# Kernel optimization log

Hardware: AMD Instinct MI355X
Metric: run time of the kernel (lower is better)

## Reference

```python
import jax, jax.numpy as jnp
import numpy as np

N_NODES = 100000
N_EDGES = 1600000
D_IN = 128
D_EMB = 128


def setup_inputs() -> dict:
    key = jax.random.key(0)
    ks = jax.random.split(key, 8)
    x = jax.random.normal(ks[0], (N_NODES, D_IN), dtype=jnp.float32)
    src = jax.random.randint(ks[1], (N_EDGES,), 0, N_NODES, dtype=jnp.int32)
    dst = jax.random.randint(ks[2], (N_EDGES,), 0, N_NODES, dtype=jnp.int32)
    # Glorot-ish init for GraphConv weights
    s = 1.0 / np.sqrt(D_EMB)
    W0 = jax.random.normal(ks[3], (D_IN, D_EMB), dtype=jnp.float32) * s
    W1 = jax.random.normal(ks[4], (D_EMB, D_EMB), dtype=jnp.float32) * s
    W2 = jax.random.normal(ks[5], (D_EMB, D_EMB), dtype=jnp.float32) * s
    b0 = jnp.zeros((D_EMB,), jnp.float32)
    b1 = jnp.zeros((D_EMB,), jnp.float32)
    b2 = jnp.zeros((D_EMB,), jnp.float32)
    return {"x": x, "src": src, "dst": dst,
            "W0": W0, "b0": b0, "W1": W1, "b1": b1, "W2": W2, "b2": b2}


def _graph_conv(h, src, dst, norm_src, norm_dst, W, b):
    # DGL GraphConv, norm='both': D_out^{-1/2} A D_in^{-1/2} H W + b
    h = h * norm_src[:, None]                       # scale src features
    m = jax.ops.segment_sum(h[src], dst, num_segments=N_NODES)  # SpMM aggregate
    m = m * norm_dst[:, None]
    return m @ W + b


def reference(x, src, dst, W0, b0, W1, b1, W2, b2):
    ones = jnp.ones((N_EDGES,), jnp.float32)
    out_deg = jax.ops.segment_sum(ones, src, num_segments=N_NODES)
    in_deg = jax.ops.segment_sum(ones, dst, num_segments=N_NODES)
    norm_src = jax.lax.rsqrt(jnp.clip(out_deg, 1.0))
    norm_dst = jax.lax.rsqrt(jnp.clip(in_deg, 1.0))

    h = x
    Ws = (W0, W1, W2)
    bs = (b0, b1, b2)
    n_layers = len(Ws)
    for layer in range(n_layers):
        h = _graph_conv(h, src, dst, norm_src, norm_dst, Ws[layer], bs[layer])
        if layer != n_layers - 1:
            h = jax.nn.relu(h)  # dropout is identity in eval mode
    return h
```

## Files before the change

### kernel.cpp

```cpp
#include <hip/hip_runtime.h>
#include <hip/hip_bf16.h>

#define N_NODES 100000
#define N_EDGES 1600000
#define D 128
#define NB 1563
#define PB 512
#define CHUNK 3125
#define SCANL (NB * PB)
#define SGRID (SCANL / 512)
#define SENT N_NODES
#define ECAP_PAD (N_EDGES + 256 * NB)
#define BCAP 2816

typedef __attribute__((ext_vector_type(8))) short bf16x8;
typedef __attribute__((ext_vector_type(4))) float f32x4;

__device__ __forceinline__ float bf2f(unsigned short u) {
    unsigned int x = ((unsigned int)u) << 16;
    return __builtin_bit_cast(float, x);
}
__device__ __forceinline__ unsigned short f2bf(float f) {
    unsigned int x = __builtin_bit_cast(unsigned int, f);
    x += 0x7fffu + ((x >> 16) & 1u);
    return (unsigned short)(x >> 16);
}
__device__ __forceinline__ void accum8(float* acc, uint4 x) {
    acc[0] += bf2f((unsigned short)x.x); acc[1] += bf2f((unsigned short)(x.x >> 16));
    acc[2] += bf2f((unsigned short)x.y); acc[3] += bf2f((unsigned short)(x.y >> 16));
    acc[4] += bf2f((unsigned short)x.z); acc[5] += bf2f((unsigned short)(x.z >> 16));
    acc[6] += bf2f((unsigned short)x.w); acc[7] += bf2f((unsigned short)(x.w >> 16));
}
__device__ __forceinline__ int XP(int b) { return ((b & 7) << 6) | (b >> 3); }

__global__ __launch_bounds__(1024) void k_pcount(const int* __restrict__ src, const int* __restrict__ dst,
                                                 int* __restrict__ cntD, int* __restrict__ cntS) {
    __shared__ int hd[NB];
    __shared__ int hs[NB];
    int t = threadIdx.x, blk = blockIdx.x;
    int col = XP(blk);
    for (int i = t; i < NB; i += 1024) { hd[i] = 0; hs[i] = 0; }
    __syncthreads();
    int base = blk * CHUNK;
    for (int i = t; i < CHUNK; i += 1024) {
        int e = base + i;
        atomicAdd(&hd[dst[e] >> 6], 1);
        atomicAdd(&hs[src[e] >> 6], 1);
    }
    __syncthreads();
    for (int i = t; i < NB; i += 1024) {
        cntD[i * PB + col] = hd[i];
        cntS[i * PB + col] = hs[i];
    }
}

__global__ void k_scanDS1(int* __restrict__ cntD, int* __restrict__ cntS, int* __restrict__ bs) {
    __shared__ int tmp[256];
    int t = threadIdx.x;
    int which = (blockIdx.x >= SGRID) ? 1 : 0;
    int blk = blockIdx.x - which * SGRID;
    int* a = which ? cntS : cntD;
    int base = blk * 512;
    int a0 = a[base + 2 * t], a1 = a[base + 2 * t + 1];
    int s = a0 + a1;
    tmp[t] = s; __syncthreads();
    for (int off = 1; off < 256; off <<= 1) {
        int x = (t >= off) ? tmp[t - off] : 0;
        __syncthreads();
        tmp[t] += x;
        __syncthreads();
    }
    int excl = tmp[t] - s;
    a[base + 2 * t] = excl;
    a[base + 2 * t + 1] = excl + a0;
    if (t == 255) bs[blockIdx.x] = tmp[255];
}

__global__ void k_scan2two(int* __restrict__ bs) {
    __shared__ int tmp[1024];
    int t = threadIdx.x;
    int base = blockIdx.x * SGRID;
    int i0 = 2 * t, i1 = 2 * t + 1;
    int a = (i0 < SGRID) ? bs[base + i0] : 0;
    int b = (i1 < SGRID) ? bs[base + i1] : 0;
    int s = a + b;
    tmp[t] = s; __syncthreads();
    for (int off = 1; off < 1024; off <<= 1) {
        int x = (t >= off) ? tmp[t - off] : 0;
        __syncthreads();
        tmp[t] += x;
        __syncthreads();
    }
    int excl = tmp[t] - s;
    if (i0 < SGRID) bs[base + i0] = excl;
    if (i1 < SGRID) bs[base + i1] = excl + a;
}


__global__ __launch_bounds__(1024) void k_pscatter(const int* __restrict__ src, const int* __restrict__ dst,
                                                   const int* __restrict__ scanD, const int* __restrict__ scanS,
                                                   const int* __restrict__ bs,
                                                   unsigned int* __restrict__ pairD, unsigned char* __restrict__ srcS) {
    __shared__ int od[NB];
    __shared__ int osx[NB];
    int t = threadIdx.x, blk = blockIdx.x;
    int col = XP(blk);
    for (int i = t; i < NB; i += 1024) {
        od[i] = scanD[i * PB + col] + bs[i];
        osx[i] = scanS[i * PB + col] + bs[SGRID + i];
    }
    __syncthreads();
    int base = blk * CHUNK;
    for (int i = t; i < CHUNK; i += 1024) {
        int e = base + i;
        int s = src[e], d = dst[e];
        int pd = atomicAdd(&od[d >> 6], 1);
        pairD[pd] = ((unsigned int)(d & 63) << 26) | (unsigned int)s;
        int ps = atomicAdd(&osx[s >> 6], 1);
        srcS[ps] = (unsigned char)(s & 63);
    }
}

__global__ __launch_bounds__(256) void k_normsrc(const unsigned char* __restrict__ srcS,
                                                 const int* __restrict__ scanS, const int* __restrict__ bs,
                                                 float* __restrict__ ns) {
    __shared__ int c[64];
    int b = blockIdx.x, t = threadIdx.x;
    if (t < 64) c[t] = 0;
    __syncthreads();
    int beg = scanS[b * PB] + bs[SGRID + b];
    int end = (b < NB - 1) ? (scanS[(b + 1) * PB] + bs[SGRID + b + 1]) : N_EDGES;
    for (int i = beg + t; i < end; i += 256) atomicAdd(&c[srcS[i]], 1);
    __syncthreads();
    if (t < 64) {
        int g = b * 64 + t;
        if (g < N_NODES) {
            int a = c[t]; if (a < 1) a = 1;
            ns[g] = rsqrtf((float)a);
        }
    }
}

__global__ __launch_bounds__(256) void k_bsortpad(const unsigned int* __restrict__ pairD,
                                                  const int* __restrict__ scanD, const int* __restrict__ bs,
                                                  int* __restrict__ esrc,
                                                  int* __restrict__ rowbeg,
                                                  int* __restrict__ degD) {
    __shared__ int cnt[64], off[64], cur[64];
    __shared__ int ptotS;
    __shared__ int stage[BCAP];
    int b = blockIdx.x, t = threadIdx.x;
    int lane = t & 63, wave = t >> 6;
    if (t < 64) cnt[t] = 0;
    __syncthreads();
    int beg = scanD[b * PB] + bs[b];
    int end = (b < NB - 1) ? (scanD[(b + 1) * PB] + bs[b + 1]) : N_EDGES;
    int n = end - beg;
    int base = beg + 256 * b;
    for (int i = t; i < n; i += 256) atomicAdd(&cnt[pairD[beg + i] >> 26], 1);
    __syncthreads();
    if (wave == 0) {
        int v = cnt[lane];
        int pc = (v + 3) & ~3;
        int x = pc;
        for (int o = 1; o < 64; o <<= 1) { int y = __shfl_up(x, o); if (lane >= o) x += y; }
        off[lane] = x - pc;
        cur[lane] = x - pc;
        if (lane == 63) ptotS = x;
    }
    __syncthreads();
    int ptot = ptotS; if (ptot > BCAP) ptot = BCAP;
    if (t < 64) {
        int g = b * 64 + t;
        if (g < N_NODES) { rowbeg[g] = base + off[t]; degD[g] = cnt[t]; }
    }
    for (int i = t; i < ptot; i += 256) stage[i] = SENT;
    __syncthreads();
    for (int i = t; i < n; i += 256) {
        unsigned int p = pairD[beg + i];
        int pos = atomicAdd(&cur[p >> 26], 1);
        if (pos < BCAP) stage[pos] = (int)(p & 0x3FFFFFFu);
    }
    __syncthreads();
    for (int i = t; i < ptot; i += 256) esrc[base + i] = stage[i];
}

__global__ void k_cvt(const float* __restrict__ x, const float* __restrict__ ns,
                      unsigned short* __restrict__ hA, unsigned short* __restrict__ hB, int n4) {
    int i = blockIdx.x * 256 + threadIdx.x;
    if (i < n4) {
        int row = i >> 5;
        float sc = ns[row];
        const float4 v = ((const float4*)x)[i];
        unsigned int lo = (unsigned int)f2bf(v.x * sc) | ((unsigned int)f2bf(v.y * sc) << 16);
        unsigned int hi = (unsigned int)f2bf(v.z * sc) | ((unsigned int)f2bf(v.w * sc) << 16);
        ((uint2*)hA)[i] = make_uint2(lo, hi);
    } else if (i < n4 + 64) {
        int j = i - n4;
        uint2 z = {0u, 0u};
        if (j < 32) ((uint2*)(hA + (size_t)SENT * D))[j] = z;
        else        ((uint2*)(hB + (size_t)SENT * D))[j - 32] = z;
    }
}

__global__ void k_transw3(const float* __restrict__ W0, const float* __restrict__ W1,
                          const float* __restrict__ W2, unsigned short* __restrict__ Wt) {
    int gid = blockIdx.x * 256 + threadIdx.x;
    if (gid >= 3 * 2048) return;
    int layer = gid >> 11;
    int di8   = gid & 2047;
    const float* W = (layer == 0) ? W0 : ((layer == 1) ? W1 : W2);
    int di   = di8 * 8;
    int lane = di8 & 63;
    int nt   = (di8 >> 6) & 7;
    int kc   = di8 >> 9;
    int quad = lane >> 4, col = lane & 15;
    unsigned short v[8];
#pragma unroll
    for (int j = 0; j < 8; j++) {
        int k = kc * 32 + quad * 8 + j;
        int nn = nt * 16 + col;
        v[j] = f2bf(W[k * 128 + nn]);
    }
    unsigned short* dp = Wt + (size_t)layer * 16384 + di;
#pragma unroll
    for (int j = 0; j < 8; j++) dp[j] = v[j];
}

__device__ __forceinline__ int aswz(int row, int byte16) {
    return row * 256 + (byte16 ^ ((row & 7) << 4));
}

__global__ __launch_bounds__(256, 8) void k_fused(const unsigned short* __restrict__ hin,
        const int* __restrict__ esrc, const int* __restrict__ rowbeg, const int* __restrict__ degD,
        const float* __restrict__ nsp,
        const unsigned short* __restrict__ Wt, const float* __restrict__ bias,
        unsigned short* __restrict__ Cb, float* __restrict__ Cf, int M) {
    __shared__ int rb[64];
    __shared__ int dgt[64];
    __shared__ unsigned short lA[64 * 128];
    int b = blockIdx.x, t = threadIdx.x;
    int lane = t & 63, wave = t >> 6;
    int sub = lane >> 4, col = lane & 15;

    if (t < 64) {
        int g = b * 64 + t;
        rb[t]  = (g < M) ? rowbeg[g] : 0;
        dgt[t] = (g < M) ? degD[g] : 0;
    }
    __syncthreads();

    for (int r = wave; r < 64; r += 4) {
        int ro = rb[r];
        int dgr = dgt[r];
        int re = ro + ((dgr + 3) & ~3);
        float acc[8];
#pragma unroll
        for (int j = 0; j < 8; j++) acc[j] = 0.f;
        int e = ro;
        while (e < re) {
            int w = e;
            int wl = w + lane;
            int idxreg = (wl < re) ? esrc[wl] : 0;
            int wend = (w + 64 < re) ? (w + 64) : re;
            for (; e + 16 <= wend; e += 16) {
                int q = e - w;
                int s0 = __shfl(idxreg, q + sub);
                int s1 = __shfl(idxreg, q + 4 + sub);
                int s2 = __shfl(idxreg, q + 8 + sub);
                int s3 = __shfl(idxreg, q + 12 + sub);
                uint4 x0 = *(const uint4*)(hin + (size_t)s0 * D + col * 8);
                uint4 x1 = *(const uint4*)(hin + (size_t)s1 * D + col * 8);
                uint4 x2 = *(const uint4*)(hin + (size_t)s2 * D + col * 8);
                uint4 x3 = *(const uint4*)(hin + (size_t)s3 * D + col * 8);
                accum8(acc, x0); accum8(acc, x1); accum8(acc, x2); accum8(acc, x3);
            }
            for (; e < wend; e += 4) {
                int q = e - w;
                int s = __shfl(idxreg, q + sub);
                uint4 x = *(const uint4*)(hin + (size_t)s * D + col * 8);
                accum8(acc, x);
            }
        }
#pragma unroll
        for (int j = 0; j < 8; j++) {
            acc[j] += __shfl_xor(acc[j], 16);
            acc[j] += __shfl_xor(acc[j], 32);
        }
        if (sub == 0) {
            int d2 = dgr; if (d2 < 1) d2 = 1;
            float s = rsqrtf((float)d2);
            uint4 o;
            o.x = (unsigned int)f2bf(acc[0] * s) | ((unsigned int)f2bf(acc[1] * s) << 16);
            o.y = (unsigned int)f2bf(acc[2] * s) | ((unsigned int)f2bf(acc[3] * s) << 16);
            o.z = (unsigned int)f2bf(acc[4] * s) | ((unsigned int)f2bf(acc[5] * s) << 16);
            o.w = (unsigned int)f2bf(acc[6] * s) | ((unsigned int)f2bf(acc[7] * s) << 16);
            *(uint4*)((char*)lA + aswz(r, col * 16)) = o;
        }
    }
    __syncthreads();

    int row0 = b * 64 + wave * 16;
    float nsv[4];
    if (Cb) {
#pragma unroll
        for (int r = 0; r < 4; r++) {
            int rr = row0 + sub * 4 + r;
            nsv[r] = (rr < M) ? nsp[rr] : 1.f;
        }
    }
#pragma unroll
    for (int half = 0; half < 2; half++) {
        f32x4 acc2[4];
#pragma unroll
        for (int i = 0; i < 4; i++) acc2[i] = (f32x4){0.f, 0.f, 0.f, 0.f};
        int lr = wave * 16 + col;
#pragma unroll
        for (int kc = 0; kc < 4; kc++) {
            bf16x8 af = *(const bf16x8*)((const char*)lA + aswz(lr, kc * 64 + sub * 16));
#pragma unroll
            for (int j = 0; j < 4; j++) {
                int nt = half * 4 + j;
                bf16x8 bfr = *(const bf16x8*)(Wt + ((size_t)(kc * 8 + nt) * 64 + lane) * 8);
                acc2[j] = __builtin_amdgcn_mfma_f32_16x16x32_bf16(af, bfr, acc2[j], 0, 0, 0);
            }
        }
#pragma unroll
        for (int j = 0; j < 4; j++) {
            int nt = half * 4 + j;
            float bv = bias[nt * 16 + col];
#pragma unroll
            for (int r = 0; r < 4; r++) {
                int rr = row0 + sub * 4 + r;
                if (rr < M) {
                    float v = acc2[j][r] + bv;
                    if (Cf) {
                        Cf[(size_t)rr * D + nt * 16 + col] = v;
                    } else {
                        v = fmaxf(v, 0.f) * nsv[r];
                        Cb[(size_t)rr * D + nt * 16 + col] = f2bf(v);
                    }
                }
            }
        }
    }
}

extern "C" void kernel_launch(void* const* d_in, const int* in_sizes, int n_in,
                              void* d_out, int out_size, void* d_ws, size_t ws_size,
                              hipStream_t stream) {
    const float* x  = (const float*)d_in[0];
    const int* src = (const int*)d_in[1];
    const int* dst = (const int*)d_in[2];
    const float* Wl[3] = {(const float*)d_in[3], (const float*)d_in[5], (const float*)d_in[7]};
    const float* Bl[3] = {(const float*)d_in[4], (const float*)d_in[6], (const float*)d_in[8]};

    const int N = N_NODES;
    const int Mpad = ((N + 63) / 64) * 64;
    const size_t HBYTES = (size_t)Mpad * D * 2;

    char* ws = (char*)d_ws;

    unsigned short* hB = (unsigned short*)ws;
    int* cntD = (int*)ws;
    int* cntS = (int*)(ws + (size_t)SCANL * 4);
    unsigned int*  pairD = (unsigned int*)(ws + (size_t)2 * SCANL * 4);
    unsigned char* srcS  = (unsigned char*)(ws + (size_t)2 * SCANL * 4 + (size_t)N_EDGES * 4);
    int* bs = (int*)(ws + (size_t)2 * SCANL * 4 + (size_t)N_EDGES * 5);

    size_t o = HBYTES;
    auto take = [&](size_t bytes) -> void* {
        o = (o + 255) & ~(size_t)255;
        void* p = ws + o;
        o += bytes;
        return p;
    };
    float* norm_src = (float*)take((size_t)N * 4);
    int*   esrc     = (int*)take((size_t)(ECAP_PAD + 256) * 4);
    int*   rowbeg   = (int*)take((size_t)N * 4);
    int*   degD     = (int*)take((size_t)N * 4);
    unsigned short* Wt = (unsigned short*)take((size_t)3 * 128 * 128 * 2);
    unsigned short* hA = (unsigned short*)take(HBYTES);

    k_pcount<<<PB, 1024, 0, stream>>>(src, dst, cntD, cntS);
    k_scanDS1<<<2 * SGRID, 256, 0, stream>>>(cntD, cntS, bs);
    k_scan2two<<<2, 1024, 0, stream>>>(bs);
    k_pscatter<<<PB, 1024, 0, stream>>>(src, dst, cntD, cntS, bs, pairD, srcS);
    k_normsrc<<<NB, 256, 0, stream>>>(srcS, cntS, bs, norm_src);
    k_bsortpad<<<NB, 256, 0, stream>>>(pairD, cntD, bs, esrc, rowbeg, degD);

    k_cvt<<<(N * 32 + 64 + 255) / 256, 256, 0, stream>>>(x, norm_src, hA, hB, N * 32);
    k_transw3<<<24, 256, 0, stream>>>(Wl[0], Wl[1], Wl[2], Wt);

    k_fused<<<NB, 256, 0, stream>>>(hA, esrc, rowbeg, degD, norm_src, Wt,         Bl[0], hB, nullptr, N);
    k_fused<<<NB, 256, 0, stream>>>(hB, esrc, rowbeg, degD, norm_src, Wt + 16384, Bl[1], hA, nullptr, N);
    k_fused<<<NB, 256, 0, stream>>>(hA, esrc, rowbeg, degD, norm_src, Wt + 32768, Bl[2], nullptr, (float*)d_out, N);
}
```

Measured before the change: 375.3 us.

## Fuse preprocessing kernels into one and prefetch next row's edge indices

Merges the source-norm, destination bucket sort, feature conversion and weight transpose kernels into a single k_prep launch, so each block converts its own 64 rows of x using norms held in shared memory. This removes three launches and a global re-read of norm_src. In the fused SpMM/GEMM kernel, each wave now loads the edge-index window for its next row before processing the current one, hiding esrc load latency. The cost is higher register pressure and more work per block in the prep kernel.

```diff
diff --git a/kernel.cpp b/kernel.cpp
--- a/kernel.cpp
+++ b/kernel.cpp
@@ -121,36 +121,77 @@
     }
 }
 
-__global__ __launch_bounds__(256) void k_normsrc(const unsigned char* __restrict__ srcS,
-                                                 const int* __restrict__ scanS, const int* __restrict__ bs,
-                                                 float* __restrict__ ns) {
+__global__ __launch_bounds__(256) void k_prep(
+        const unsigned int* __restrict__ pairD, const unsigned char* __restrict__ srcS,
+        const int* __restrict__ scanD, const int* __restrict__ scanS, const int* __restrict__ bs,
+        const float* __restrict__ x,
+        const float* __restrict__ W0, const float* __restrict__ W1, const float* __restrict__ W2,
+        int* __restrict__ esrc, int* __restrict__ rowbeg, int* __restrict__ degD,
+        float* __restrict__ norm_src, unsigned short* __restrict__ Wt,
+        unsigned short* __restrict__ hA, unsigned short* __restrict__ hB) {
     __shared__ int c[64];
-    int b = blockIdx.x, t = threadIdx.x;
-    if (t < 64) c[t] = 0;
-    __syncthreads();
-    int beg = scanS[b * PB] + bs[SGRID + b];
-    int end = (b < NB - 1) ? (scanS[(b + 1) * PB] + bs[SGRID + b + 1]) : N_EDGES;
-    for (int i = beg + t; i < end; i += 256) atomicAdd(&c[srcS[i]], 1);
-    __syncthreads();
-    if (t < 64) {
-        int g = b * 64 + t;
-        if (g < N_NODES) {
-            int a = c[t]; if (a < 1) a = 1;
-            ns[g] = rsqrtf((float)a);
-        }
-    }
-}
-
-__global__ __launch_bounds__(256) void k_bsortpad(const unsigned int* __restrict__ pairD,
-                                                  const int* __restrict__ scanD, const int* __restrict__ bs,
-                                                  int* __restrict__ esrc,
-                                                  int* __restrict__ rowbeg,
-                                                  int* __restrict__ degD) {
+    __shared__ float nsl[64];
     __shared__ int cnt[64], off[64], cur[64];
     __shared__ int ptotS;
     __shared__ int stage[BCAP];
     int b = blockIdx.x, t = threadIdx.x;
     int lane = t & 63, wave = t >> 6;
+
+    if (b < 24) {
+        int gid = b * 256 + t;
+        int layer = gid >> 11;
+        int di8   = gid & 2047;
+        const float* W = (layer == 0) ? W0 : ((layer == 1) ? W1 : W2);
+        int di   = di8 * 8;
+        int wl   = di8 & 63;
+        int nt   = (di8 >> 6) & 7;
+        int kc   = di8 >> 9;
+        int quad = wl >> 4, wcol = wl & 15;
+        unsigned short v[8];
+#pragma unroll
+        for (int j = 0; j < 8; j++) {
+            int k = kc * 32 + quad * 8 + j;
+            v[j] = f2bf(W[k * 128 + nt * 16 + wcol]);
+        }
+        unsigned short* dp = Wt + (size_t)layer * 16384 + di;
+#pragma unroll
+        for (int j = 0; j < 8; j++) dp[j] = v[j];
+    }
+    if (b == 0 && t < 32) {
+        uint4 z = {0u, 0u, 0u, 0u};
+        if (t < 16) ((uint4*)(hA + (size_t)SENT * D))[t] = z;
+        else        ((uint4*)(hB + (size_t)SENT * D))[t - 16] = z;
+    }
+
+    if (t < 64) c[t] = 0;
+    __syncthreads();
+    int begS = scanS[b * PB] + bs[SGRID + b];
+    int endS = (b < NB - 1) ? (scanS[(b + 1) * PB] + bs[SGRID + b + 1]) : N_EDGES;
+    for (int i = begS + t; i < endS; i += 256) atomicAdd(&c[srcS[i]], 1);
+    __syncthreads();
+    if (t < 64) {
+        int g = b * 64 + t;
+        float nv = 1.f;
+        if (g < N_NODES) {
+            int a = c[t]; if (a < 1) a = 1;
+            nv = rsqrtf((float)a);
+            norm_src[g] = nv;
+        }
+        nsl[t] = nv;
+    }
+    __syncthreads();
+
+    for (int i = t; i < 2048; i += 256) {
+        int row = b * 64 + (i >> 5);
+        if (row < N_NODES) {
+            float sc = nsl[i >> 5];
+            const float4 v = ((const float4*)x)[(size_t)row * 32 + (i & 31)];
+            unsigned int lo = (unsigned int)f2bf(v.x * sc) | ((unsigned int)f2bf(v.y * sc) << 16);
+            unsigned int hi = (unsigned int)f2bf(v.z * sc) | ((unsigned int)f2bf(v.w * sc) << 16);
+            ((uint2*)hA)[(size_t)row * 32 + (i & 31)] = make_uint2(lo, hi);
+        }
+    }
+
     if (t < 64) cnt[t] = 0;
     __syncthreads();
     int beg = scanD[b * PB] + bs[b];
@@ -162,11 +203,11 @@
     if (wave == 0) {
         int v = cnt[lane];
         int pc = (v + 3) & ~3;
-        int x = pc;
-        for (int o = 1; o < 64; o <<= 1) { int y = __shfl_up(x, o); if (lane >= o) x += y; }
-        off[lane] = x - pc;
-        cur[lane] = x - pc;
-        if (lane == 63) ptotS = x;
+        int xx = pc;
+        for (int o = 1; o < 64; o <<= 1) { int y = __shfl_up(xx, o); if (lane >= o) xx += y; }
+        off[lane] = xx - pc;
+        cur[lane] = xx - pc;
+        if (lane == 63) ptotS = xx;
     }
     __syncthreads();
     int ptot = ptotS; if (ptot > BCAP) ptot = BCAP;
@@ -183,48 +224,6 @@
     }
     __syncthreads();
     for (int i = t; i < ptot; i += 256) esrc[base + i] = stage[i];
-}
-
-__global__ void k_cvt(const float* __restrict__ x, const float* __restrict__ ns,
-                      unsigned short* __restrict__ hA, unsigned short* __restrict__ hB, int n4) {
-    int i = blockIdx.x * 256 + threadIdx.x;
-    if (i < n4) {
-        int row = i >> 5;
-        float sc = ns[row];
-        const float4 v = ((const float4*)x)[i];
-        unsigned int lo = (unsigned int)f2bf(v.x * sc) | ((unsigned int)f2bf(v.y * sc) << 16);
-        unsigned int hi = (unsigned int)f2bf(v.z * sc) | ((unsigned int)f2bf(v.w * sc) << 16);
-        ((uint2*)hA)[i] = make_uint2(lo, hi);
-    } else if (i < n4 + 64) {
-        int j = i - n4;
-        uint2 z = {0u, 0u};
-        if (j < 32) ((uint2*)(hA + (size_t)SENT * D))[j] = z;
-        else        ((uint2*)(hB + (size_t)SENT * D))[j - 32] = z;
-    }
-}
-
-__global__ void k_transw3(const float* __restrict__ W0, const float* __restrict__ W1,
-                          const float* __restrict__ W2, unsigned short* __restrict__ Wt) {
-    int gid = blockIdx.x * 256 + threadIdx.x;
-    if (gid >= 3 * 2048) return;
-    int layer = gid >> 11;
-    int di8   = gid & 2047;
-    const float* W = (layer == 0) ? W0 : ((layer == 1) ? W1 : W2);
-    int di   = di8 * 8;
-    int lane = di8 & 63;
-    int nt   = (di8 >> 6) & 7;
-    int kc   = di8 >> 9;
-    int quad = lane >> 4, col = lane & 15;
-    unsigned short v[8];
-#pragma unroll
-    for (int j = 0; j < 8; j++) {
-        int k = kc * 32 + quad * 8 + j;
-        int nn = nt * 16 + col;
-        v[j] = f2bf(W[k * 128 + nn]);
-    }
-    unsigned short* dp = Wt + (size_t)layer * 16384 + di;
-#pragma unroll
-    for (int j = 0; j < 8; j++) dp[j] = v[j];
 }
 
 __device__ __forceinline__ int aswz(int row, int byte16) {
@@ -250,19 +249,24 @@
     }
     __syncthreads();
 
-    for (int r = wave; r < 64; r += 4) {
-        int ro = rb[r];
-        int dgr = dgt[r];
-        int re = ro + ((dgr + 3) & ~3);
+    int r = wave;
+    int ro = rb[r], dgr = dgt[r];
+    int re = ro + ((dgr + 3) & ~3);
+    int idxreg = (ro + lane < re) ? esrc[ro + lane] : 0;
+    for (int k = 0; k < 16; k++, r += 4) {
+        int nro = 0, ndgr = 0, nre = 0, nidx = 0;
+        if (k < 15) {
+            nro = rb[r + 4]; ndgr = dgt[r + 4];
+            nre = nro + ((ndgr + 3) & ~3);
+            nidx = (nro + lane < nre) ? esrc[nro + lane] : 0;
+        }
         float acc[8];
 #pragma unroll
         for (int j = 0; j < 8; j++) acc[j] = 0.f;
-        int e = ro;
-        while (e < re) {
-            int w = e;
-            int wl = w + lane;
-            int idxreg = (wl < re) ? esrc[wl] : 0;
-            int wend = (w + 64 < re) ? (w + 64) : re;
+        int w = ro;
+        int wend = (w + 64 < re) ? (w + 64) : re;
+        int e = w;
+        while (true) {
             for (; e + 16 <= wend; e += 16) {
                 int q = e - w;
                 int s0 = __shfl(idxreg, q + sub);
@@ -281,6 +285,10 @@
                 uint4 x = *(const uint4*)(hin + (size_t)s * D + col * 8);
                 accum8(acc, x);
             }
+            if (wend >= re) break;
+            w = wend;
+            idxreg = (w + lane < re) ? esrc[w + lane] : 0;
+            wend = (w + 64 < re) ? (w + 64) : re;
         }
 #pragma unroll
         for (int j = 0; j < 8; j++) {
@@ -297,6 +305,7 @@
             o.w = (unsigned int)f2bf(acc[6] * s) | ((unsigned int)f2bf(acc[7] * s) << 16);
             *(uint4*)((char*)lA + aswz(r, col * 16)) = o;
         }
+        ro = nro; dgr = ndgr; re = nre; idxreg = nidx;
     }
     __syncthreads();
 
@@ -304,9 +313,9 @@
     float nsv[4];
     if (Cb) {
 #pragma unroll
-        for (int r = 0; r < 4; r++) {
-            int rr = row0 + sub * 4 + r;
-            nsv[r] = (rr < M) ? nsp[rr] : 1.f;
+        for (int rr4 = 0; rr4 < 4; rr4++) {
+            int rr = row0 + sub * 4 + rr4;
+            nsv[rr4] = (rr < M) ? nsp[rr] : 1.f;
         }
     }
 #pragma unroll
@@ -330,14 +339,14 @@
             int nt = half * 4 + j;
             float bv = bias[nt * 16 + col];
 #pragma unroll
-            for (int r = 0; r < 4; r++) {
-                int rr = row0 + sub * 4 + r;
+            for (int rr4 = 0; rr4 < 4; rr4++) {
+                int rr = row0 + sub * 4 + rr4;
                 if (rr < M) {
-                    float v = acc2[j][r] + bv;
+                    float v = acc2[j][rr4] + bv;
                     if (Cf) {
                         Cf[(size_t)rr * D + nt * 16 + col] = v;
                     } else {
-                        v = fmaxf(v, 0.f) * nsv[r];
+                        v = fmaxf(v, 0.f) * nsv[rr4];
                         Cb[(size_t)rr * D + nt * 16 + col] = f2bf(v);
                     }
                 }
@@ -386,11 +395,9 @@
     k_scanDS1<<<2 * SGRID, 256, 0, stream>>>(cntD, cntS, bs);
     k_scan2two<<<2, 1024, 0, stream>>>(bs);
     k_pscatter<<<PB, 1024, 0, stream>>>(src, dst, cntD, cntS, bs, pairD, srcS);
-    k_normsrc<<<NB, 256, 0, stream>>>(srcS, cntS, bs, norm_src);
-    k_bsortpad<<<NB, 256, 0, stream>>>(pairD, cntD, bs, esrc, rowbeg, degD);
-
-    k_cvt<<<(N * 32 + 64 + 255) / 256, 256, 0, stream>>>(x, norm_src, hA, hB, N * 32);
-    k_transw3<<<24, 256, 0, stream>>>(Wl[0], Wl[1], Wl[2], Wt);
+    k_prep<<<NB, 256, 0, stream>>>(pairD, srcS, cntD, cntS, bs, x,
+                                   Wl[0], Wl[1], Wl[2],
+                                   esrc, rowbeg, degD, norm_src, Wt, hA, hB);
 
     k_fused<<<NB, 256, 0, stream>>>(hA, esrc, rowbeg, degD, norm_src, Wt,         Bl[0], hB, nullptr, N);
     k_fused<<<NB, 256, 0, stream>>>(hB, esrc, rowbeg, degD, norm_src, Wt + 16384, Bl[1], hA, nullptr, N);
```

Measured after the change: 370.5 us. No clear change (-1.3%).
